# Optimization experiments

Hardware: AMD Instinct MI355X
Metric: run time of the kernel (lower is better)

Reference implementation:

```python
import jax, jax.numpy as jnp
import numpy as np

NUM_NODES = 100000
NUM_EDGES = 1600000
NUM_GRAPHS = 1000
NUM_REP = 16
R_DIM = 16
N_SCALARS = 16
N_CLASSES = 6
N_LAYERS = 3
L_MAX = 1
EPS = 1e-8


def get_rot(v):
    """2x2 SO(2) rotation from 2D vector angle, L_max=1. v:[n,2] -> [n,1,2,2]."""
    theta = jnp.arctan2(v[:, 1], v[:, 0])
    c, s = jnp.cos(theta), jnp.sin(theta)
    R = jnp.stack([jnp.stack([c, -s], -1), jnp.stack([s, c], -1)], -2)  # [n,2,2]
    return R[:, None]  # [n, L_max=1, 2, 2]


def bessel(d, number=R_DIM, end=1.0):
    """Bessel radial basis sqrt(2/end)*sin(n*pi*d/end)/d. d:[E] -> [E,number]."""
    n = jnp.arange(1, number + 1, dtype=d.dtype)
    d_safe = d[:, None] + EPS
    return jnp.sqrt(2.0 / end) * jnp.sin(n * jnp.pi * d[:, None] / end) / d_safe


def seg_sum(x, idx, n):
    return jax.ops.segment_sum(x, idx, num_segments=n)


def setup_inputs() -> dict:
    key = jax.random.key(0)
    ks = jax.random.split(key, 20)
    pos = jax.random.normal(ks[0], (NUM_NODES, 2), dtype=jnp.float32)
    edge_index = jax.random.randint(ks[1], (2, NUM_EDGES), 0, NUM_NODES)
    batch = jnp.sort(jax.random.randint(ks[2], (NUM_NODES,), 0, NUM_GRAPHS))
    s = 0.1
    return {
        "pos": pos,
        "W_emb_rot": s * jax.random.normal(ks[3], (NUM_REP, L_MAX, 2), jnp.float32),
        "w_s_emb": s * jax.random.normal(ks[4], (N_SCALARS,), jnp.float32),
        "b_s_emb": jnp.zeros((N_SCALARS,), jnp.float32),
        "Wg": s * jax.random.normal(ks[5], (N_LAYERS, R_DIM, NUM_REP), jnp.float32),
        "bg": jnp.zeros((N_LAYERS, NUM_REP), jnp.float32),
        "Wmix": s * jax.random.normal(ks[6], (N_LAYERS, NUM_REP, NUM_REP), jnp.float32),
        "Wgate": s * jax.random.normal(ks[7], (N_LAYERS, N_SCALARS, NUM_REP), jnp.float32),
        "bgate": jnp.zeros((N_LAYERS, NUM_REP), jnp.float32),
        "Ws1": s * jax.random.normal(ks[8], (N_LAYERS, N_SCALARS + R_DIM, N_SCALARS), jnp.float32),
        "bs1": jnp.zeros((N_LAYERS, N_SCALARS), jnp.float32),
        "W1": s * jax.random.normal(ks[9], (N_SCALARS + NUM_REP * L_MAX * 2, 3 * (N_SCALARS + NUM_REP * L_MAX * 2)), jnp.float32),
        "b1": jnp.zeros((3 * (N_SCALARS + NUM_REP * L_MAX * 2),), jnp.float32),
        "W2": s * jax.random.normal(ks[10], (3 * (N_SCALARS + NUM_REP * L_MAX * 2), N_CLASSES), jnp.float32),
        "b2": jnp.zeros((N_CLASSES,), jnp.float32),
        "edge_index": edge_index,
        "batch": batch,
    }


def reference(pos, W_emb_rot, w_s_emb, b_s_emb, Wg, bg, Wmix, Wgate, bgate,
              Ws1, bs1, W1, b1, W2, b2, edge_index, batch):
    N = pos.shape[0]
    # --- geometry under no_grad in torch ---
    posg = jax.lax.stop_gradient(pos)
    cnt = seg_sum(jnp.ones((N,), posg.dtype), batch, NUM_GRAPHS)
    mean = seg_sum(posg, batch, NUM_GRAPHS) / jnp.maximum(cnt, 1.0)[:, None]
    posg = posg - mean[batch]
    rot_theta = get_rot(posg)                        # [N,1,2,2]
    row, col = edge_index[0], edge_index[1]
    edge_vec = posg[row] - posg[col]                 # [E,2]
    rot = get_rot(edge_vec)                          # [E,1,2,2]
    dist = jnp.linalg.norm(edge_vec, axis=1)         # [E]

    dist_emb = bessel(dist)                          # [E,r_dim]

    # --- edge embedding -> node features ---
    e_rot = jnp.einsum('eklm,jkm->ejkl', rot, W_emb_rot)      # [E,rep,1,2]
    deg = jnp.maximum(seg_sum(jnp.ones((row.shape[0],), pos.dtype), row, N), 1.0)
    x_rot = seg_sum(e_rot, row, N) / deg[:, None, None, None]  # [N,rep,1,2]
    d_mean = seg_sum(dist, row, N) / deg
    x_s = jax.nn.leaky_relu(d_mean[:, None] * w_s_emb[None, :] + b_s_emb)  # [N,ns]

    rot_inv = jnp.swapaxes(rot, -1, -2)
    # --- EqBlocks: gather -> rotate-in -> radial mix -> rotate-out -> scatter ---
    for i in range(N_LAYERS):
        local = jnp.einsum('eklm,ejkm->ejkl', rot_inv, x_rot[col])   # [E,rep,1,2]
        g = dist_emb @ Wg[i] + bg[i]                                 # [E,rep]
        local = jnp.einsum('ij,ejkl->eikl', Wmix[i], local) * g[:, :, None, None]
        msg = jnp.einsum('eklm,ejkm->ejkl', rot, local)              # [E,rep,1,2]
        agg = seg_sum(msg, row, N) / deg[:, None, None, None]
        gate = jax.nn.sigmoid(x_s @ Wgate[i] + bgate[i])             # [N,rep]
        x_rot = x_rot + agg * gate[:, :, None, None]
        msg_s = jax.nn.leaky_relu(
            jnp.concatenate([x_s[col], dist_emb], axis=1) @ Ws1[i] + bs1[i])
        x_s = x_s + seg_sum(msg_s, row, N) / deg[:, None]

    # --- SO2OutU (faithful to given source) ---
    rot_theta_inv = jnp.swapaxes(rot_theta, -1, -2)                  # [N,1,2,2]
    x_out = jnp.einsum('njkm,nkml->njkl', x_rot, rot_theta_inv)      # [N,rep,1,2]
    x_cat = jnp.concatenate([x_s, x_out.reshape(N, -1)], axis=1)    # [N,48]
    u = jax.nn.leaky_relu(x_cat @ W1 + b1) @ W2 + b2                 # [N,n_classes]
    return seg_sum(u, batch, NUM_GRAPHS)                             # [G,n_classes]
```

## Files before the change

### kernel.cpp

```cpp
#include <hip/hip_runtime.h>
#include <hip/hip_fp16.h>
#include <math.h>

#define NREP 16
#define RDIM 16
#define NS   16
#define NC   6
#define H1   144
#define DBINS 64
#define TILE 4096
#define NBMAX 512
#define P2CAP 10240

static __device__ __forceinline__ float leaky(float v) { return v > 0.0f ? v : 0.01f * v; }

__global__ void __launch_bounds__(256) k_gsum_bhist(
    const float* __restrict__ pos, const int* __restrict__ batch, int N,
    float* __restrict__ gsum, float* __restrict__ gcnt,
    const int* __restrict__ ei, int E, int* __restrict__ bhist) {
  int t = threadIdx.x;
  __shared__ int h[NBMAX];
  for (int i = t; i < NBMAX; i += 256) h[i] = 0;
  __syncthreads();
  int base = blockIdx.x * TILE;
  int lim = min(base + TILE, E);
  for (int j = base + t; j < lim; j += 256) atomicAdd(&h[ei[j] >> 8], 1);
  __syncthreads();
  for (int i = t; i < NBMAX; i += 256)
    if (h[i] > 0) atomicAdd(&bhist[i], h[i]);

  __shared__ float bx[320], by[320], bc[320];
  int start = blockIdx.x * 256;
  if (start >= N) return;
  int n = start + t;
  int b0 = batch[min(start, N - 1)];
  int span = batch[min(start + 255, N - 1)] - b0;
  bool useLds = (span < 320);
  if (useLds) {
    for (int i = t; i <= span; i += 256) { bx[i] = 0.f; by[i] = 0.f; bc[i] = 0.f; }
    __syncthreads();
    if (n < N) {
      int rb = batch[n] - b0;
      atomicAdd(&bx[rb], pos[2 * n + 0]);
      atomicAdd(&by[rb], pos[2 * n + 1]);
      atomicAdd(&bc[rb], 1.0f);
    }
    __syncthreads();
    for (int i = t; i <= span; i += 256) {
      if (bc[i] != 0.0f) {
        atomicAdd(&gsum[2 * (b0 + i) + 0], bx[i]);
        atomicAdd(&gsum[2 * (b0 + i) + 1], by[i]);
        atomicAdd(&gcnt[b0 + i], bc[i]);
      }
    }
  } else if (n < N) {
    int b = batch[n];
    atomicAdd(&gsum[2 * b + 0], pos[2 * n + 0]);
    atomicAdd(&gsum[2 * b + 1], pos[2 * n + 1]);
    atomicAdd(&gcnt[b], 1.0f);
  }
}

__global__ void __launch_bounds__(256) k_center_bscan(
    const float* __restrict__ pos, const int* __restrict__ batch, int N, int E,
    const float* __restrict__ gsum, const float* __restrict__ gcnt,
    float* __restrict__ posc, float* __restrict__ cthn, float* __restrict__ sthn,
    const int* __restrict__ bhist, int* __restrict__ bbase, int* __restrict__ bcur, int NB) {
  int t = threadIdx.x;
  if (blockIdx.x == 0) {
    __shared__ int s[NBMAX];
    int v0 = (t < NB) ? bhist[t] : 0;
    int v1 = (t + 256 < NB) ? bhist[t + 256] : 0;
    s[t] = v0; s[t + 256] = v1;
    __syncthreads();
    for (int o = 1; o < NBMAX; o <<= 1) {
      int a0 = (t >= o) ? s[t - o] : 0;
      int a1 = s[t + 256 - o];
      __syncthreads();
      s[t] += a0; s[t + 256] += a1;
      __syncthreads();
    }
    if (t < NB)       { int ex = s[t] - v0;       bbase[t] = ex;       bcur[t] = ex; }
    if (t + 256 < NB) { int ex = s[t + 256] - v1; bbase[t + 256] = ex; bcur[t + 256] = ex; }
    if (t == 0) bbase[NB] = E;
  }
  int i = blockIdx.x * 256 + t;
  if (i < N) {
    int b = batch[i];
    float invc = 1.0f / fmaxf(gcnt[b], 1.0f);
    float px = pos[2 * i + 0] - gsum[2 * b + 0] * invc;
    float py = pos[2 * i + 1] - gsum[2 * b + 1] * invc;
    posc[2 * i + 0] = px;
    posc[2 * i + 1] = py;
    float r = sqrtf(px * px + py * py);
    if (r > 0.0f) { cthn[i] = px / r; sthn[i] = py / r; }
    else          { cthn[i] = 1.0f;  sthn[i] = 0.0f; }
  }
}

__global__ void __launch_bounds__(256) k_part1(
    const int* __restrict__ ei, int E,
    int* __restrict__ bcur, long long* __restrict__ ebuf) {
  __shared__ int hist[NBMAX], lofs[NBMAX], gbase[NBMAX], pc[NBMAX];
  __shared__ long long stg[TILE];
  __shared__ unsigned short bkt[TILE];
  int t = threadIdx.x;
  int base = blockIdx.x * TILE;
  int cntt = min(TILE, E - base);
  for (int i = t; i < NBMAX; i += 256) { hist[i] = 0; pc[i] = 0; }
  __syncthreads();
  int r[16], c[16];
#pragma unroll
  for (int i = 0; i < 16; i++) {
    int e = base + t + i * 256;
    r[i] = -1;
    if (e < E) {
      r[i] = ei[e];
      c[i] = ei[E + e];
      atomicAdd(&hist[r[i] >> 8], 1);
    }
  }
  __syncthreads();
  lofs[t] = hist[t]; lofs[t + 256] = hist[t + 256];
  __syncthreads();
  for (int o = 1; o < NBMAX; o <<= 1) {
    int a0 = (t >= o) ? lofs[t - o] : 0;
    int a1 = lofs[t + 256 - o];
    __syncthreads();
    lofs[t] += a0; lofs[t + 256] += a1;
    __syncthreads();
  }
  int e0 = lofs[t] - hist[t], e1 = lofs[t + 256] - hist[t + 256];
  __syncthreads();
  lofs[t] = e0; lofs[t + 256] = e1;
  __syncthreads();
  for (int i = t; i < NBMAX; i += 256)
    if (hist[i] > 0) gbase[i] = atomicAdd(&bcur[i], hist[i]);
  __syncthreads();
#pragma unroll
  for (int i = 0; i < 16; i++) {
    if (r[i] >= 0) {
      int b = r[i] >> 8;
      int l = lofs[b] + atomicAdd(&pc[b], 1);
      stg[l] = ((long long)r[i] << 32) | (unsigned int)c[i];
      bkt[l] = (unsigned short)b;
    }
  }
  __syncthreads();
  for (int j = t; j < cntt; j += 256) {
    int b = bkt[j];
    ebuf[gbase[b] + (j - lofs[b])] = stg[j];
  }
}

__global__ void __launch_bounds__(256) k_part2i(
    const int* __restrict__ bbase, int N, int E,
    const long long* __restrict__ ebuf,
    const float* __restrict__ posc,
    int* __restrict__ off, int* __restrict__ cnt, int* __restrict__ dhist,
    int* __restrict__ adj, float2* __restrict__ spc,
    const float* __restrict__ Wer, const float* __restrict__ wse, const float* __restrict__ bse,
    const float* __restrict__ Wmix, const float* __restrict__ Ws1, const float* __restrict__ bs1,
    const float* __restrict__ Wgate, const float* __restrict__ bgate,
    float* __restrict__ xr, float* __restrict__ xs, uint2* __restrict__ yzg) {
  __shared__ int lcnt[256], loff[256], lcur[256];
  __shared__ float lC[256], lS[256], lD[256], lpx[256], lpy[256];
  __shared__ int lh[DBINS];
  __shared__ int ladj[P2CAP];
  __shared__ unsigned char lrow[P2CAP];
  int t = threadIdx.x;
  int b = blockIdx.x;
  int r0 = b << 8;
  int abeg = bbase[b];
  int aend = bbase[b + 1];
  int sz = aend - abeg;
  bool haveRow = (r0 + t < N);
  lcnt[t] = 0;
  lC[t] = 0.f; lS[t] = 0.f; lD[t] = 0.f;
  if (t < DBINS) lh[t] = 0;
  if (haveRow) { lpx[t] = posc[2 * (r0 + t)]; lpy[t] = posc[2 * (r0 + t) + 1]; }
  __syncthreads();
  for (int j = abeg + t; j < aend; j += 256)
    atomicAdd(&lcnt[(int)(ebuf[j] >> 32) - r0], 1);
  __syncthreads();
  int v = lcnt[t];
  loff[t] = v;
  __syncthreads();
  for (int o = 1; o < 256; o <<= 1) {
    int u = (t >= o) ? loff[t - o] : 0;
    __syncthreads();
    loff[t] += u;
    __syncthreads();
  }
  int myoff = loff[t] - v;
  __syncthreads();
  loff[t] = myoff;
  lcur[t] = myoff;
  if (haveRow) {
    off[r0 + t] = abeg + myoff;
    cnt[r0 + t] = v;
    atomicAdd(&lh[min(v, DBINS - 1)], 1);
  }
  if (t == 0 && r0 + 256 >= N) off[N] = E;
  __syncthreads();
  if (t < DBINS && lh[t] > 0) atomicAdd(&dhist[t], lh[t]);
  if (sz <= P2CAP) {
    for (int j = abeg + t; j < aend; j += 256) {
      long long p = ebuf[j];
      int cl = (int)(unsigned int)(p & 0xffffffffLL);
      int rr = (int)(p >> 32) - r0;
      int l = atomicAdd(&lcur[rr], 1);
      ladj[l] = cl;
      lrow[l] = (unsigned char)rr;
    }
    __syncthreads();
    for (int k = t; k < sz; k += 256) {
      int cl = ladj[k];
      int rr = lrow[k];
      adj[abeg + k] = cl;
      float dx = lpx[rr] - posc[2 * cl + 0];
      float dy = lpy[rr] - posc[2 * cl + 1];
      float d = sqrtf(dx * dx + dy * dy);
      float sp, cp;
      sincospif(d, &sp, &cp);
      spc[abeg + k] = make_float2(1.41421356237309515f * sp / (d + 1e-8f), 2.0f * cp);
      float invd = (d > 0.f) ? 1.f / d : 0.f;
      atomicAdd(&lC[rr], (d > 0.f) ? dx * invd : 1.0f);
      atomicAdd(&lS[rr], dy * invd);
      atomicAdd(&lD[rr], d);
    }
  } else {
    for (int j = abeg + t; j < aend; j += 256) {
      long long p = ebuf[j];
      int cl = (int)(unsigned int)(p & 0xffffffffLL);
      int rr = (int)(p >> 32) - r0;
      int l = abeg + atomicAdd(&lcur[rr], 1);
      adj[l] = cl;
      float dx = lpx[rr] - posc[2 * cl + 0];
      float dy = lpy[rr] - posc[2 * cl + 1];
      float d = sqrtf(dx * dx + dy * dy);
      float sp, cp;
      sincospif(d, &sp, &cp);
      spc[l] = make_float2(1.41421356237309515f * sp / (d + 1e-8f), 2.0f * cp);
      float invd = (d > 0.f) ? 1.f / d : 0.f;
      atomicAdd(&lC[rr], (d > 0.f) ? dx * invd : 1.0f);
      atomicAdd(&lS[rr], dy * invd);
      atomicAdd(&lD[rr], d);
    }
  }
  __syncthreads();
  int r = t & 15;
  float wmxn[16], wsan[16], wgtn[16];
#pragma unroll
  for (int q = 0; q < 16; q++) wmxn[q] = Wmix[r * 16 + q];
#pragma unroll
  for (int q = 0; q < 16; q++) wsan[q] = Ws1[q * 16 + r];
#pragma unroll
  for (int q = 0; q < 16; q++) wgtn[q] = Wgate[q * 16 + r];
  float w0 = Wer[2 * r], w1 = Wer[2 * r + 1];
  for (int round = 0; round < 16; round++) {
    int node = (round << 4) + (t >> 4);
    int n = r0 + node;
    if (n >= N) continue;
    float id = 1.0f / fmaxf((float)lcnt[node], 1.0f);
    float C = lC[node] * id, S = lS[node] * id, dm = lD[node] * id;
    float2 x;
    x.x = C * w0 - S * w1;
    x.y = S * w0 + C * w1;
    ((float2*)xr)[(size_t)n * 16 + r] = x;
    float s_new = leaky(dm * wse[r] + bse[r]);
    xs[(size_t)n * 16 + r] = s_new;
    float y0 = 0.f, y1 = 0.f;
    float z = bs1[r], gtn = bgate[r];
#pragma unroll
    for (int j = 0; j < 16; j++) {
      float xj0 = __shfl(x.x, j, 16);
      float xj1 = __shfl(x.y, j, 16);
      float sj  = __shfl(s_new, j, 16);
      y0 += wmxn[j] * xj0;
      y1 += wmxn[j] * xj1;
      z  += wsan[j] * sj;
      gtn += wgtn[j] * sj;
    }
    gtn = 1.0f / (1.0f + __expf(-gtn));
    __half2 hA = __floats2half2_rn(y0, y1);
    __half2 hB = __floats2half2_rn(z, gtn);
    uint2 w2;
    w2.x = *(unsigned int*)&hA;
    w2.y = *(unsigned int*)&hB;
    yzg[(size_t)n * 16 + r] = w2;
  }
}

__global__ void k_permfill(int N, const int* __restrict__ cnt,
                           const int* __restrict__ dhist,
                           int* __restrict__ dcur, int* __restrict__ perm) {
  __shared__ int sd[DBINS], dbase[DBINS];
  __shared__ int lh[DBINS], base[DBINS];
  int t = threadIdx.x;
  int dv = 0;
  if (t < DBINS) { dv = dhist[t]; sd[t] = dv; lh[t] = 0; }
  __syncthreads();
  for (int o = 1; o < DBINS; o <<= 1) {
    int u = (t >= o && t < DBINS) ? sd[t - o] : 0;
    __syncthreads();
    if (t < DBINS) sd[t] += u;
    __syncthreads();
  }
  if (t < DBINS) dbase[t] = sd[t] - dv;
  __syncthreads();
  int i = blockIdx.x * 1024 + t;
  int b = 0, lr = 0;
  if (i < N) {
    b = min(cnt[i], DBINS - 1);
    lr = atomicAdd(&lh[b], 1);
  }
  __syncthreads();
  if (t < DBINS && lh[t] > 0) base[t] = dbase[t] + atomicAdd(&dcur[t], lh[t]);
  __syncthreads();
  if (i < N) perm[base[b] + lr] = i;
}

__global__ void __launch_bounds__(256) k_layer(
    int N, const int* __restrict__ off,
    const int* __restrict__ adj, const float2* __restrict__ spc,
    const uint2* __restrict__ yzg, const int* __restrict__ perm,
    const float* __restrict__ Wg, const float* __restrict__ bg,
    const float* __restrict__ Ws1,
    float* xr, float* xs,
    int write_next, uint2* __restrict__ yzg_out,
    const float* __restrict__ Wmixn, const float* __restrict__ Ws1n,
    const float* __restrict__ bs1n,
    const float* __restrict__ Wgaten, const float* __restrict__ bgaten) {
  int idx = blockIdx.x * 256 + threadIdx.x;
  int g = idx >> 4, r = idx & 15;
  if (g >= N) return;
  int n = perm[g];
  float wg[16], ws[16];
#pragma unroll
  for (int q = 0; q < 16; q++) wg[q] = Wg[q * 16 + r];
#pragma unroll
  for (int q = 0; q < 16; q++) ws[q] = Ws1[(16 + q) * 16 + r];
  float bgr = bg[r];

  int a = off[n], bnd = off[n + 1];
  float acc0 = 0.f, acc1 = 0.f, accs = 0.f;
  if (a < bnd) {
    int last = bnd - 1;
    int    c0 = adj[a];               float2 p0 = spc[a];
    int    c1 = adj[min(a + 1, last)]; float2 p1 = spc[min(a + 1, last)];
    int    cn = adj[min(a + 2, last)]; float2 p2 = spc[min(a + 2, last)];
    uint2 Y0 = yzg[(c0 << 4) + r];
    uint2 Y1 = yzg[(c1 << 4) + r];
    int k = a;
    for (; k + 3 < bnd; k++) {
      int c3 = adj[k + 3];
      float2 p3 = spc[k + 3];
      uint2 Y2 = yzg[(cn << 4) + r];
      float skm1 = 0.f, sk = p0.x, c2 = p0.y;
      float g1 = bgr, dot = 0.f;
#pragma unroll
      for (int q = 0; q < RDIM; q++) {
        g1  = __builtin_fmaf(sk, wg[q], g1);
        dot = __builtin_fmaf(sk, ws[q], dot);
        float sn = __builtin_fmaf(c2, sk, -skm1);
        skm1 = sk; sk = sn;
      }
      float2 f01 = __half22float2(*(__half2*)&Y0.x);
      float2 fzg = __half22float2(*(__half2*)&Y0.y);
      acc0 = __builtin_fmaf(g1, f01.x, acc0);
      acc1 = __builtin_fmaf(g1, f01.y, acc1);
      accs += leaky(dot + fzg.x);
      c0 = c1; p0 = p1; c1 = cn; p1 = p2; cn = c3; p2 = p3; Y0 = Y1; Y1 = Y2;
    }
    for (; k < bnd; k++) {
      uint2 Y2 = Y1;
      if (k + 2 < bnd) Y2 = yzg[(cn << 4) + r];
      float skm1 = 0.f, sk = p0.x, c2 = p0.y;
      float g1 = bgr, dot = 0.f;
#pragma unroll
      for (int q = 0; q < RDIM; q++) {
        g1  = __builtin_fmaf(sk, wg[q], g1);
        dot = __builtin_fmaf(sk, ws[q], dot);
        float sn = __builtin_fmaf(c2, sk, -skm1);
        skm1 = sk; sk = sn;
      }
      float2 f01 = __half22float2(*(__half2*)&Y0.x);
      float2 fzg = __half22float2(*(__half2*)&Y0.y);
      acc0 = __builtin_fmaf(g1, f01.x, acc0);
      acc1 = __builtin_fmaf(g1, f01.y, acc1);
      accs += leaky(dot + fzg.x);
      c0 = c1; p0 = p1; c1 = cn; p1 = p2; Y0 = Y1; Y1 = Y2;
    }
  }
  float id = 1.0f / fmaxf((float)(bnd - a), 1.0f);
  uint2 Yg = yzg[(n << 4) + r];
  float gt = __half22float2(*(__half2*)&Yg.y).y;
  float2* xr2 = (float2*)xr;
  float2 x = xr2[(n << 4) + r];
  x.x += acc0 * id * gt;
  x.y += acc1 * id * gt;
  xr2[(n << 4) + r] = x;
  float s_new = xs[(n << 4) + r] + accs * id;
  xs[(n << 4) + r] = s_new;

  if (write_next) {
    float wmxn[16], wsan[16], wgtn[16];
#pragma unroll
    for (int q = 0; q < 16; q++) wmxn[q] = Wmixn[r * 16 + q];
#pragma unroll
    for (int q = 0; q < 16; q++) wsan[q] = Ws1n[q * 16 + r];
#pragma unroll
    for (int q = 0; q < 16; q++) wgtn[q] = Wgaten[q * 16 + r];
    float y0 = 0.f, y1 = 0.f;
    float z = bs1n[r], gtn = bgaten[r];
#pragma unroll
    for (int j = 0; j < 16; j++) {
      float xj0 = __shfl(x.x, j, 16);
      float xj1 = __shfl(x.y, j, 16);
      float sj  = __shfl(s_new, j, 16);
      y0 += wmxn[j] * xj0;
      y1 += wmxn[j] * xj1;
      z  += wsan[j] * sj;
      gtn += wgtn[j] * sj;
    }
    gtn = 1.0f / (1.0f + __expf(-gtn));
    __half2 hA = __floats2half2_rn(y0, y1);
    __half2 hB = __floats2half2_rn(z, gtn);
    uint2 w2;
    w2.x = *(unsigned int*)&hA;
    w2.y = *(unsigned int*)&hB;
    yzg_out[(n << 4) + r] = w2;
  }
}

__global__ void __launch_bounds__(128) k_final(
    int N, const float* __restrict__ xr, const float* __restrict__ xs,
    const float* __restrict__ cthn, const float* __restrict__ sthn,
    const int* __restrict__ batch,
    const float* __restrict__ W1, const float* __restrict__ b1,
    const float* __restrict__ W2, const float* __restrict__ b2,
    float* __restrict__ out) {
  __shared__ float obin[320 * 6];
  int t = threadIdx.x;
  int start = blockIdx.x * 128;
  int n = start + t;
  int b0 = batch[min(start, N - 1)];
  int span = batch[min(start + 127, N - 1)] - b0;
  bool useLds = (span < 320);
  if (useLds) for (int i = t; i < (span + 1) * 6; i += 128) obin[i] = 0.f;
  __syncthreads();

  float u[NC];
  bool act = (n < N);
  if (act) {
    float xc[48];
    const float4* xs4 = (const float4*)(xs + (size_t)n * NS);
#pragma unroll
    for (int j = 0; j < 4; j++) {
      float4 v = xs4[j];
      xc[4 * j + 0] = v.x; xc[4 * j + 1] = v.y; xc[4 * j + 2] = v.z; xc[4 * j + 3] = v.w;
    }
    float c = cthn[n], s = sthn[n];
    const float4* xr4 = (const float4*)(xr + (size_t)n * 32);
#pragma unroll
    for (int j = 0; j < 8; j++) {
      float4 v = xr4[j];
      xc[16 + 4 * j + 0] = c * v.x - s * v.y;
      xc[16 + 4 * j + 1] = s * v.x + c * v.y;
      xc[16 + 4 * j + 2] = c * v.z - s * v.w;
      xc[16 + 4 * j + 3] = s * v.z + c * v.w;
    }
#pragma unroll
    for (int q = 0; q < NC; q++) u[q] = b2[q];
    for (int h = 0; h < H1; h += 4) {
      float a0 = b1[h + 0], a1 = b1[h + 1], a2 = b1[h + 2], a3 = b1[h + 3];
#pragma unroll
      for (int q = 0; q < 48; q++) {
        float4 w = *(const float4*)(W1 + (size_t)q * H1 + h);
        float x = xc[q];
        a0 = __builtin_fmaf(x, w.x, a0);
        a1 = __builtin_fmaf(x, w.y, a1);
        a2 = __builtin_fmaf(x, w.z, a2);
        a3 = __builtin_fmaf(x, w.w, a3);
      }
      a0 = leaky(a0); a1 = leaky(a1); a2 = leaky(a2); a3 = leaky(a3);
#pragma unroll
      for (int q = 0; q < NC; q++)
        u[q] += a0 * W2[(h + 0) * 6 + q] + a1 * W2[(h + 1) * 6 + q]
              + a2 * W2[(h + 2) * 6 + q] + a3 * W2[(h + 3) * 6 + q];
    }
  }
  if (useLds) {
    if (act) {
      int rb = batch[n] - b0;
#pragma unroll
      for (int q = 0; q < NC; q++) atomicAdd(&obin[rb * 6 + q], u[q]);
    }
    __syncthreads();
    for (int i = t; i < (span + 1) * 6; i += 128) atomicAdd(&out[b0 * 6 + i], obin[i]);
  } else if (act) {
    int b = batch[n];
#pragma unroll
    for (int q = 0; q < NC; q++) atomicAdd(&out[b * 6 + q], u[q]);
  }
}

extern "C" void kernel_launch(void* const* d_in, const int* in_sizes, int n_in,
                              void* d_out, int out_size, void* d_ws, size_t ws_size,
                              hipStream_t stream) {
  const float* pos   = (const float*)d_in[0];
  const float* Wer   = (const float*)d_in[1];
  const float* wse   = (const float*)d_in[2];
  const float* bse   = (const float*)d_in[3];
  const float* Wg    = (const float*)d_in[4];
  const float* bg    = (const float*)d_in[5];
  const float* Wmix  = (const float*)d_in[6];
  const float* Wgate = (const float*)d_in[7];
  const float* bgate = (const float*)d_in[8];
  const float* Ws1   = (const float*)d_in[9];
  const float* bs1   = (const float*)d_in[10];
  const float* W1    = (const float*)d_in[11];
  const float* b1    = (const float*)d_in[12];
  const float* W2    = (const float*)d_in[13];
  const float* b2    = (const float*)d_in[14];
  const int*   ei    = (const int*)d_in[15];
  const int*   batch = (const int*)d_in[16];
  float* out = (float*)d_out;

  int N = in_sizes[0] / 2;
  int E = in_sizes[15] / 2;
  int G = out_size / NC;
  int NB = (N + 255) / 256;

  float* W = (float*)d_ws;
  size_t o = 0;
  float* gsum   = W + o; o += (size_t)2 * G;
  float* gcnt   = W + o; o += (size_t)G;
  int*   bhist  = (int*)(W + o); o += (size_t)NBMAX;
  int*   dhist  = (int*)(W + o); o += (size_t)DBINS;
  int*   dcur   = (int*)(W + o); o += (size_t)DBINS;
  size_t zero_bytes = o * 4;
  o = (o + 3) & ~(size_t)3;
  float* posc   = W + o; o += (size_t)2 * N;
  float* cthn   = W + o; o += (size_t)N;
  float* sthn   = W + o; o += (size_t)N;
  int*   off    = (int*)(W + o); o += (size_t)N + 1; o = (o + 3) & ~(size_t)3;
  int*   bbase  = (int*)(W + o); o += (size_t)NBMAX + 1;
  int*   bcur   = (int*)(W + o); o += (size_t)NBMAX;
  int*   cnt    = (int*)(W + o); o += (size_t)N;
  int*   perm   = (int*)(W + o); o += (size_t)N; o = (o + 3) & ~(size_t)3;
  int*   adj    = (int*)(W + o); o += (size_t)E; o = (o + 1) & ~(size_t)1;
  float2* spc   = (float2*)(W + o); o += (size_t)2 * E;
  long long* ebuf = (long long*)spc;
  uint2* yzgA   = (uint2*)(W + o); o += (size_t)32 * N;
  uint2* yzgB   = (uint2*)(W + o); o += (size_t)32 * N;
  float* xr     = W + o; o += (size_t)N * 32;
  float* xs     = W + o; o += (size_t)N * 16;
  (void)ws_size;

  hipMemsetAsync(d_ws, 0, zero_bytes, stream);
  hipMemsetAsync(d_out, 0, (size_t)out_size * 4, stream);

  int nbN  = (N + 255) / 256;
  int nbT  = (E + TILE - 1) / TILE;
  int nbG  = nbT > nbN ? nbT : nbN;
  int nbN16 = ((size_t)N * 16 + 255) / 256;
  int nbP  = (N + 1023) / 1024;
  int nbF  = (N + 127) / 128;

  k_gsum_bhist<<<nbG, 256, 0, stream>>>(pos, batch, N, gsum, gcnt, ei, E, bhist);
  k_center_bscan<<<nbN, 256, 0, stream>>>(pos, batch, N, E, gsum, gcnt,
                                          posc, cthn, sthn, bhist, bbase, bcur, NB);
  k_part1<<<nbT, 256, 0, stream>>>(ei, E, bcur, ebuf);
  k_part2i<<<NB, 256, 0, stream>>>(bbase, N, E, ebuf, posc,
                                   off, cnt, dhist, adj, spc,
                                   Wer, wse, bse, Wmix, Ws1, bs1, Wgate, bgate,
                                   xr, xs, yzgA);
  k_permfill<<<nbP, 1024, 0, stream>>>(N, cnt, dhist, dcur, perm);

  k_layer<<<nbN16, 256, 0, stream>>>(N, off, adj, spc, yzgA, perm,
                                     Wg, bg, Ws1, xr, xs,
                                     1, yzgB,
                                     Wmix + 256, Ws1 + 512, bs1 + 16, Wgate + 256, bgate + 16);
  k_layer<<<nbN16, 256, 0, stream>>>(N, off, adj, spc, yzgB, perm,
                                     Wg + 256, bg + 16, Ws1 + 512, xr, xs,
                                     1, yzgA,
                                     Wmix + 512, Ws1 + 1024, bs1 + 32, Wgate + 512, bgate + 32);
  k_layer<<<nbN16, 256, 0, stream>>>(N, off, adj, spc, yzgA, perm,
                                     Wg + 512, bg + 32, Ws1 + 1024, xr, xs,
                                     0, yzgB,
                                     Wmix, Ws1, bs1, Wgate, bgate);

  k_final<<<nbF, 128, 0, stream>>>(N, xr, xs, cthn, sthn, batch, W1, b1, W2, b2, out);
}
```

Before: 446.2 us.

## Split edge partition from per-edge geometry and node init into separate kernel

The partition kernel now only builds the CSR adjacency. A new kernel assigns 16 threads per node to compute per-edge distance and Bessel terms, reduce the mean direction and distance with shuffles, and produce the initial node features and layer-0 projections. This drops the shared-memory float atomics and the large per-block LDS footprint of the fused kernel, which should raise occupancy and parallelism. The cost is an extra kernel launch and a second read of adj and off from global memory.

```diff
diff --git a/kernel.cpp b/kernel.cpp
--- a/kernel.cpp
+++ b/kernel.cpp
@@ -153,21 +153,14 @@
   }
 }
 
-__global__ void __launch_bounds__(256) k_part2i(
+__global__ void __launch_bounds__(256) k_part2(
     const int* __restrict__ bbase, int N, int E,
     const long long* __restrict__ ebuf,
-    const float* __restrict__ posc,
     int* __restrict__ off, int* __restrict__ cnt, int* __restrict__ dhist,
-    int* __restrict__ adj, float2* __restrict__ spc,
-    const float* __restrict__ Wer, const float* __restrict__ wse, const float* __restrict__ bse,
-    const float* __restrict__ Wmix, const float* __restrict__ Ws1, const float* __restrict__ bs1,
-    const float* __restrict__ Wgate, const float* __restrict__ bgate,
-    float* __restrict__ xr, float* __restrict__ xs, uint2* __restrict__ yzg) {
+    int* __restrict__ adj) {
   __shared__ int lcnt[256], loff[256], lcur[256];
-  __shared__ float lC[256], lS[256], lD[256], lpx[256], lpy[256];
   __shared__ int lh[DBINS];
   __shared__ int ladj[P2CAP];
-  __shared__ unsigned char lrow[P2CAP];
   int t = threadIdx.x;
   int b = blockIdx.x;
   int r0 = b << 8;
@@ -176,9 +169,7 @@
   int sz = aend - abeg;
   bool haveRow = (r0 + t < N);
   lcnt[t] = 0;
-  lC[t] = 0.f; lS[t] = 0.f; lD[t] = 0.f;
   if (t < DBINS) lh[t] = 0;
-  if (haveRow) { lpx[t] = posc[2 * (r0 + t)]; lpy[t] = posc[2 * (r0 + t) + 1]; }
   __syncthreads();
   for (int j = abeg + t; j < aend; j += 256)
     atomicAdd(&lcnt[(int)(ebuf[j] >> 32) - r0], 1);
@@ -209,47 +200,68 @@
       long long p = ebuf[j];
       int cl = (int)(unsigned int)(p & 0xffffffffLL);
       int rr = (int)(p >> 32) - r0;
-      int l = atomicAdd(&lcur[rr], 1);
-      ladj[l] = cl;
-      lrow[l] = (unsigned char)rr;
-    }
-    __syncthreads();
-    for (int k = t; k < sz; k += 256) {
-      int cl = ladj[k];
-      int rr = lrow[k];
-      adj[abeg + k] = cl;
-      float dx = lpx[rr] - posc[2 * cl + 0];
-      float dy = lpy[rr] - posc[2 * cl + 1];
-      float d = sqrtf(dx * dx + dy * dy);
-      float sp, cp;
-      sincospif(d, &sp, &cp);
-      spc[abeg + k] = make_float2(1.41421356237309515f * sp / (d + 1e-8f), 2.0f * cp);
-      float invd = (d > 0.f) ? 1.f / d : 0.f;
-      atomicAdd(&lC[rr], (d > 0.f) ? dx * invd : 1.0f);
-      atomicAdd(&lS[rr], dy * invd);
-      atomicAdd(&lD[rr], d);
-    }
+      ladj[atomicAdd(&lcur[rr], 1)] = cl;
+    }
+    __syncthreads();
+    for (int j = t; j < sz; j += 256) adj[abeg + j] = ladj[j];
   } else {
     for (int j = abeg + t; j < aend; j += 256) {
       long long p = ebuf[j];
       int cl = (int)(unsigned int)(p & 0xffffffffLL);
       int rr = (int)(p >> 32) - r0;
-      int l = abeg + atomicAdd(&lcur[rr], 1);
-      adj[l] = cl;
-      float dx = lpx[rr] - posc[2 * cl + 0];
-      float dy = lpy[rr] - posc[2 * cl + 1];
-      float d = sqrtf(dx * dx + dy * dy);
-      float sp, cp;
-      sincospif(d, &sp, &cp);
-      spc[l] = make_float2(1.41421356237309515f * sp / (d + 1e-8f), 2.0f * cp);
-      float invd = (d > 0.f) ? 1.f / d : 0.f;
-      atomicAdd(&lC[rr], (d > 0.f) ? dx * invd : 1.0f);
-      atomicAdd(&lS[rr], dy * invd);
-      atomicAdd(&lD[rr], d);
-    }
-  }
-  __syncthreads();
-  int r = t & 15;
+      adj[abeg + atomicAdd(&lcur[rr], 1)] = cl;
+    }
+  }
+}
+
+__global__ void __launch_bounds__(256) k_init16(
+    int N, const int* __restrict__ off, const int* __restrict__ adj,
+    const float* __restrict__ posc, float2* __restrict__ spc,
+    const float* __restrict__ Wer, const float* __restrict__ wse, const float* __restrict__ bse,
+    const float* __restrict__ Wmix, const float* __restrict__ Ws1, const float* __restrict__ bs1,
+    const float* __restrict__ Wgate, const float* __restrict__ bgate,
+    float* __restrict__ xr, float* __restrict__ xs, uint2* __restrict__ yzg) {
+  int idx = blockIdx.x * 256 + threadIdx.x;
+  int n = idx >> 4, r = idx & 15;
+  if (n >= N) return;
+  int a = off[n], b = off[n + 1];
+  float px = posc[2 * n + 0], py = posc[2 * n + 1];
+  float C = 0.f, S = 0.f, D = 0.f;
+  for (int k = a + r; k < b; k += 16) {
+    int cl = adj[k];
+    float dx = px - posc[2 * cl + 0];
+    float dy = py - posc[2 * cl + 1];
+    float d = sqrtf(dx * dx + dy * dy);
+    float sp, cp;
+    sincospif(d, &sp, &cp);
+    float spp = 1.41421356237309515f * sp / (d + 1e-8f);
+    spc[k] = make_float2(spp, 2.0f * cp);
+    if (d > 0.0f) {
+      float inv = 1.0f / d;
+      C += dx * inv;
+      S += dy * inv;
+    } else {
+      C += 1.0f;
+    }
+    D += d;
+  }
+#pragma unroll
+  for (int o = 1; o < 16; o <<= 1) {
+    C += __shfl_xor(C, o, 16);
+    S += __shfl_xor(S, o, 16);
+    D += __shfl_xor(D, o, 16);
+  }
+  float id = 1.0f / fmaxf((float)(b - a), 1.0f);
+  C *= id; S *= id;
+  float dm = D * id;
+  float w0 = Wer[2 * r], w1 = Wer[2 * r + 1];
+  float2 x;
+  x.x = C * w0 - S * w1;
+  x.y = S * w0 + C * w1;
+  ((float2*)xr)[(size_t)n * 16 + r] = x;
+  float s_new = leaky(dm * wse[r] + bse[r]);
+  xs[(size_t)n * 16 + r] = s_new;
+
   float wmxn[16], wsan[16], wgtn[16];
 #pragma unroll
   for (int q = 0; q < 16; q++) wmxn[q] = Wmix[r * 16 + q];
@@ -257,39 +269,25 @@
   for (int q = 0; q < 16; q++) wsan[q] = Ws1[q * 16 + r];
 #pragma unroll
   for (int q = 0; q < 16; q++) wgtn[q] = Wgate[q * 16 + r];
-  float w0 = Wer[2 * r], w1 = Wer[2 * r + 1];
-  for (int round = 0; round < 16; round++) {
-    int node = (round << 4) + (t >> 4);
-    int n = r0 + node;
-    if (n >= N) continue;
-    float id = 1.0f / fmaxf((float)lcnt[node], 1.0f);
-    float C = lC[node] * id, S = lS[node] * id, dm = lD[node] * id;
-    float2 x;
-    x.x = C * w0 - S * w1;
-    x.y = S * w0 + C * w1;
-    ((float2*)xr)[(size_t)n * 16 + r] = x;
-    float s_new = leaky(dm * wse[r] + bse[r]);
-    xs[(size_t)n * 16 + r] = s_new;
-    float y0 = 0.f, y1 = 0.f;
-    float z = bs1[r], gtn = bgate[r];
-#pragma unroll
-    for (int j = 0; j < 16; j++) {
-      float xj0 = __shfl(x.x, j, 16);
-      float xj1 = __shfl(x.y, j, 16);
-      float sj  = __shfl(s_new, j, 16);
-      y0 += wmxn[j] * xj0;
-      y1 += wmxn[j] * xj1;
-      z  += wsan[j] * sj;
-      gtn += wgtn[j] * sj;
-    }
-    gtn = 1.0f / (1.0f + __expf(-gtn));
-    __half2 hA = __floats2half2_rn(y0, y1);
-    __half2 hB = __floats2half2_rn(z, gtn);
-    uint2 w2;
-    w2.x = *(unsigned int*)&hA;
-    w2.y = *(unsigned int*)&hB;
-    yzg[(size_t)n * 16 + r] = w2;
-  }
+  float y0 = 0.f, y1 = 0.f;
+  float z = bs1[r], gtn = bgate[r];
+#pragma unroll
+  for (int j = 0; j < 16; j++) {
+    float xj0 = __shfl(x.x, j, 16);
+    float xj1 = __shfl(x.y, j, 16);
+    float sj  = __shfl(s_new, j, 16);
+    y0 += wmxn[j] * xj0;
+    y1 += wmxn[j] * xj1;
+    z  += wsan[j] * sj;
+    gtn += wgtn[j] * sj;
+  }
+  gtn = 1.0f / (1.0f + __expf(-gtn));
+  __half2 hA = __floats2half2_rn(y0, y1);
+  __half2 hB = __floats2half2_rn(z, gtn);
+  uint2 w2;
+  w2.x = *(unsigned int*)&hA;
+  w2.y = *(unsigned int*)&hB;
+  yzg[(size_t)n * 16 + r] = w2;
 }
 
 __global__ void k_permfill(int N, const int* __restrict__ cnt,
@@ -573,10 +571,10 @@
   k_center_bscan<<<nbN, 256, 0, stream>>>(pos, batch, N, E, gsum, gcnt,
                                           posc, cthn, sthn, bhist, bbase, bcur, NB);
   k_part1<<<nbT, 256, 0, stream>>>(ei, E, bcur, ebuf);
-  k_part2i<<<NB, 256, 0, stream>>>(bbase, N, E, ebuf, posc,
-                                   off, cnt, dhist, adj, spc,
-                                   Wer, wse, bse, Wmix, Ws1, bs1, Wgate, bgate,
-                                   xr, xs, yzgA);
+  k_part2<<<NB, 256, 0, stream>>>(bbase, N, E, ebuf, off, cnt, dhist, adj);
+  k_init16<<<nbN16, 256, 0, stream>>>(N, off, adj, posc, spc, Wer, wse, bse,
+                                      Wmix, Ws1, bs1, Wgate, bgate,
+                                      xr, xs, yzgA);
   k_permfill<<<nbP, 1024, 0, stream>>>(N, cnt, dhist, dcur, perm);
 
   k_layer<<<nbN16, 256, 0, stream>>>(N, off, adj, spc, yzgA, perm,
```

Result: faster. 412.5 us (-7.6%).
